# Kernel tuning notes

Measured on AMD Instinct MI355X. Metric: run time of the kernel, lower is better.

## Reference

```python
import jax, jax.numpy as jnp
import numpy as np

N = 2048
EMBED_DIM = 64
N_SUBJ, N_REL, N_OBJ = 16, 9, 16


def setup_inputs() -> dict:
    key = jax.random.key(0)
    ks = jax.random.split(key, 16)
    scale = 0.05  # keep sigmoid unsaturated
    return {
        "subj_idx": jax.random.randint(ks[0], (N,), 0, N_SUBJ, dtype=jnp.int32),
        "rel_idx": jax.random.randint(ks[1], (N,), 0, N_REL, dtype=jnp.int32),
        "obj_idx": jax.random.randint(ks[2], (N,), 0, N_OBJ, dtype=jnp.int32),
        "subj_table": jax.random.normal(ks[3], (N_SUBJ, EMBED_DIM), jnp.float32),
        "rel_table": jax.random.normal(ks[4], (N_REL, EMBED_DIM), jnp.float32),
        "obj_table": jax.random.normal(ks[5], (N_OBJ, EMBED_DIM), jnp.float32),
        "proj_w": jax.random.normal(ks[6], (EMBED_DIM, 3 * EMBED_DIM), jnp.float32) * scale,
        "proj_b": jax.random.normal(ks[7], (EMBED_DIM,), jnp.float32) * scale,
        "w1": jax.random.normal(ks[8], (EMBED_DIM, 2 * EMBED_DIM), jnp.float32) * scale,
        "b1": jax.random.normal(ks[9], (EMBED_DIM,), jnp.float32) * scale,
        "w2": jax.random.normal(ks[10], (32, EMBED_DIM), jnp.float32) * scale,
        "b2": jax.random.normal(ks[11], (32,), jnp.float32) * scale,
        "w3": jax.random.normal(ks[12], (1, 32), jnp.float32) * scale,
        "b3": jax.random.normal(ks[13], (1,), jnp.float32) * scale,
    }


def reference(subj_idx, rel_idx, obj_idx, subj_table, rel_table, obj_table,
              proj_w, proj_b, w1, b1, w2, b2, w3, b3):
    # --- ClaimEmbedder.embed, batched over all N claims ---
    # combined [N, 3*D] = cat(subj, rel, obj) embeddings; proj -> [N, D]
    combined = jnp.concatenate(
        [subj_table[subj_idx], rel_table[rel_idx], obj_table[obj_idx]], axis=-1)
    e = combined @ proj_w.T + proj_b  # [N, D]

    # --- conflict_scorer over all ordered pairs (i, j) ---
    # Linear(2D -> D) on cat(e_i, e_j) == e_i @ W1a.T + e_j @ W1b.T + b1
    d = e.shape[-1]
    w1a, w1b = w1[:, :d], w1[:, d:]
    hi = e @ w1a.T          # [N, D] contribution of left claim
    hj = e @ w1b.T          # [N, D] contribution of right claim
    h = jax.nn.relu(hi[:, None, :] + hj[None, :, :] + b1)  # [N, N, D]
    # Dropout(0.1) is identity in eval / no_grad inference.
    h2 = jax.nn.relu(jnp.einsum('ijd,kd->ijk', h, w2) + b2)  # [N, N, 32]
    scores = jax.nn.sigmoid(jnp.einsum('ijk,k->ij', h2, w3[0]) + b3[0])  # [N, N]
    # Only pairs with i < j are scored in the original nested loop.
    return jnp.triu(scores, k=1)
```

## Files before the change

kernel.cpp:

```cpp
#include <hip/hip_runtime.h>
#include <hip/hip_bf16.h>

#define NROWS 2048

typedef __attribute__((ext_vector_type(4))) float f32x4;
typedef _Float16 f16x2 __attribute__((ext_vector_type(2)));
typedef _Float16 f16x8 __attribute__((ext_vector_type(8)));
typedef __fp16 fp16x2_raw __attribute__((ext_vector_type(2)));

union H8 { f16x8 v; f16x2 h2[4]; };

static __device__ __forceinline__ f32x4 vmax0(f32x4 a) {
    return __builtin_elementwise_max(a, (f32x4)0.f);
}
static __device__ __forceinline__ f16x8 hmax0(f16x8 a) {
    return __builtin_elementwise_max(a, (f16x8)(_Float16)0.f);
}
static __device__ __forceinline__ f16x2 pkrtz(float a, float b) {
    union { fp16x2_raw r; f16x2 f; } c;
    c.r = __builtin_amdgcn_cvt_pkrtz(a, b);
    return c.f;
}

#define TJ_OFF   2688
#define H16_OFF  5376

__global__ __launch_bounds__(256) void tab_kernel(
    const float* __restrict__ subj_table, const float* __restrict__ rel_table,
    const float* __restrict__ obj_table,
    const float* __restrict__ proj_w, const float* __restrict__ proj_b,
    const float* __restrict__ w1, const float* __restrict__ b1,
    float* __restrict__ ws)
{
    __shared__ float et[64];
    const int b = blockIdx.x;
    const int side = b & 1;
    const int r = b >> 1;
    const int tid = threadIdx.x;
    const int lane = tid & 63;
    const int w = tid >> 6;

    if (r == 41) {
        if (tid < 64) et[tid] = proj_b[tid];
    } else {
        const float* src; int off;
        if (r < 16)      { src = subj_table + r * 64;        off = 0;   }
        else if (r < 25) { src = rel_table + (r - 16) * 64;  off = 64;  }
        else             { src = obj_table + (r - 25) * 64;  off = 128; }
        const float sv = src[lane];
        #pragma unroll
        for (int t = 0; t < 4; ++t) {
            const int d0 = w * 16 + t * 4;
            float p0 = sv * proj_w[(d0 + 0) * 192 + off + lane];
            float p1 = sv * proj_w[(d0 + 1) * 192 + off + lane];
            float p2 = sv * proj_w[(d0 + 2) * 192 + off + lane];
            float p3 = sv * proj_w[(d0 + 3) * 192 + off + lane];
            #pragma unroll
            for (int m = 1; m < 64; m <<= 1) {
                p0 += __shfl_xor(p0, m, 64);
                p1 += __shfl_xor(p1, m, 64);
                p2 += __shfl_xor(p2, m, 64);
                p3 += __shfl_xor(p3, m, 64);
            }
            if (lane == 0) {
                et[d0 + 0] = p0; et[d0 + 1] = p1;
                et[d0 + 2] = p2; et[d0 + 3] = p3;
            }
        }
    }
    __syncthreads();

    float* dst = ws + (side ? TJ_OFF : 0);
    const float sv2 = et[lane];
    const int woff = side * 64;
    #pragma unroll
    for (int t = 0; t < 4; ++t) {
        const int d0 = w * 16 + t * 4;
        float p0 = sv2 * w1[(d0 + 0) * 128 + woff + lane];
        float p1 = sv2 * w1[(d0 + 1) * 128 + woff + lane];
        float p2 = sv2 * w1[(d0 + 2) * 128 + woff + lane];
        float p3 = sv2 * w1[(d0 + 3) * 128 + woff + lane];
        #pragma unroll
        for (int m = 1; m < 64; m <<= 1) {
            p0 += __shfl_xor(p0, m, 64);
            p1 += __shfl_xor(p1, m, 64);
            p2 += __shfl_xor(p2, m, 64);
            p3 += __shfl_xor(p3, m, 64);
        }
        if (lane == 0) {
            const bool cst = (side == 0) && (r == 41);
            dst[r * 64 + d0 + 0] = p0 + (cst ? b1[d0 + 0] : 0.f);
            dst[r * 64 + d0 + 1] = p1 + (cst ? b1[d0 + 1] : 0.f);
            dst[r * 64 + d0 + 2] = p2 + (cst ? b1[d0 + 2] : 0.f);
            dst[r * 64 + d0 + 3] = p3 + (cst ? b1[d0 + 3] : 0.f);
        }
    }
}

__global__ __launch_bounds__(256) void hgather_kernel(
    const int* __restrict__ subj_idx, const int* __restrict__ rel_idx,
    const int* __restrict__ obj_idx, float* __restrict__ ws)
{
    _Float16* hi16 = (_Float16*)(ws + H16_OFF);
    _Float16* hj16 = hi16 + NROWS * 64;
    const float* TI = ws;
    const float* TJ = ws + TJ_OFF;

    const int t = threadIdx.x;
    const int n = blockIdx.x * 32 + (t >> 3);
    const int c = (t & 7) * 8;

    const int s = subj_idx[n];
    const int r = 16 + rel_idx[n];
    const int o = 25 + obj_idx[n];

    const f32x4 v0 = *(const f32x4*)(TI + s * 64 + c)
                   + *(const f32x4*)(TI + r * 64 + c)
                   + *(const f32x4*)(TI + o * 64 + c)
                   + *(const f32x4*)(TI + 41 * 64 + c);
    const f32x4 v1 = *(const f32x4*)(TI + s * 64 + c + 4)
                   + *(const f32x4*)(TI + r * 64 + c + 4)
                   + *(const f32x4*)(TI + o * 64 + c + 4)
                   + *(const f32x4*)(TI + 41 * 64 + c + 4);
    H8 hp;
    hp.h2[0] = pkrtz(v0[0], v0[1]); hp.h2[1] = pkrtz(v0[2], v0[3]);
    hp.h2[2] = pkrtz(v1[0], v1[1]); hp.h2[3] = pkrtz(v1[2], v1[3]);
    *(f16x8*)&hi16[(size_t)n * 64 + c] = hp.v;

    const f32x4 u0 = *(const f32x4*)(TJ + s * 64 + c)
                   + *(const f32x4*)(TJ + r * 64 + c)
                   + *(const f32x4*)(TJ + o * 64 + c)
                   + *(const f32x4*)(TJ + 41 * 64 + c);
    const f32x4 u1 = *(const f32x4*)(TJ + s * 64 + c + 4)
                   + *(const f32x4*)(TJ + r * 64 + c + 4)
                   + *(const f32x4*)(TJ + o * 64 + c + 4)
                   + *(const f32x4*)(TJ + 41 * 64 + c + 4);
    H8 hq;
    hq.h2[0] = pkrtz(u0[0], u0[1]); hq.h2[1] = pkrtz(u0[2], u0[3]);
    hq.h2[2] = pkrtz(u1[0], u1[1]); hq.h2[3] = pkrtz(u1[2], u1[3]);
    *(f16x8*)&hj16[(size_t)n * 64 + c] = hq.v;
}

#define PSTR 68

__global__ __launch_bounds__(256, 4) void pair_kernel(
    const float* __restrict__ ws,
    const float* __restrict__ w2, const float* __restrict__ b2,
    const float* __restrict__ w3, const float* __restrict__ b3,
    float* __restrict__ out)
{
    const int bx = blockIdx.x, by = blockIdx.y;
    const int i0 = by * 32, j0 = bx * 32;
    const int tid = threadIdx.x;

    if (bx < by) {
        const float4 z = {0.f, 0.f, 0.f, 0.f};
        ((float4*)(out + (size_t)(i0 + (tid >> 3)) * NROWS + j0))[tid & 7] = z;
        return;
    }

    __shared__ float part[4 * 16 * PSTR];

    const _Float16* hi16 = (const _Float16*)(ws + H16_OFF);
    const _Float16* hj16 = hi16 + NROWS * 64;

    const int lane = tid & 63;
    const int wid  = tid >> 6;
    const int col  = lane & 15;
    const int quad = lane >> 4;
    const int wj   = wid & 1;
    const int wi   = wid >> 1;

    const _Float16* hjr = hj16 + (size_t)(j0 + wj * 16 + col) * 64 + quad * 8;
    const f16x8 hj0 = *(const f16x8*)(hjr);
    const f16x8 hj1 = *(const f16x8*)(hjr + 32);

    H8 wf[2][2];
    #pragma unroll
    for (int ch = 0; ch < 2; ++ch)
        #pragma unroll
        for (int ks = 0; ks < 2; ++ks) {
            const f32x4* wr = (const f32x4*)(w2 + (ch * 16 + col) * 64 + ks * 32 + quad * 8);
            const f32x4 w0 = wr[0], w1v = wr[1];
            wf[ch][ks].h2[0] = pkrtz(w0[0], w0[1]);
            wf[ch][ks].h2[1] = pkrtz(w0[2], w0[3]);
            wf[ch][ks].h2[2] = pkrtz(w1v[0], w1v[1]);
            wf[ch][ks].h2[3] = pkrtz(w1v[2], w1v[3]);
        }
    const f32x4 b2A = *(const f32x4*)(b2 + quad * 4);
    const f32x4 b2B = *(const f32x4*)(b2 + 16 + quad * 4);
    const f32x4 w3A = *(const f32x4*)(w3 + quad * 4);
    const f32x4 w3B = *(const f32x4*)(w3 + 16 + quad * 4);
    const float b3v = b3[0];

    float* mypart = &part[wid * 16 * PSTR];
    const _Float16* hibase = hi16 + (size_t)(i0 + wi * 16) * 64 + quad * 8;

    #pragma unroll 8
    for (int it = 0; it < 16; ++it) {
        const f16x8 x0 = *(const f16x8*)(hibase + it * 64);
        const f16x8 x1 = *(const f16x8*)(hibase + it * 64 + 32);

        const f16x8 f0 = hmax0(x0 + hj0);
        const f16x8 f1 = hmax0(x1 + hj1);

        f32x4 accA = __builtin_amdgcn_mfma_f32_16x16x32_f16(wf[0][0].v, f0, b2A, 0, 0, 0);
        accA       = __builtin_amdgcn_mfma_f32_16x16x32_f16(wf[0][1].v, f1, accA, 0, 0, 0);
        f32x4 accB = __builtin_amdgcn_mfma_f32_16x16x32_f16(wf[1][0].v, f0, b2B, 0, 0, 0);
        accB       = __builtin_amdgcn_mfma_f32_16x16x32_f16(wf[1][1].v, f1, accB, 0, 0, 0);

        const f32x4 ra = vmax0(accA);
        const f32x4 rb = vmax0(accB);
        const f32x4 t4 = ra * w3A + rb * w3B;
        mypart[it * PSTR + quad * 16 + col] = (t4[0] + t4[1]) + (t4[2] + t4[3]);
    }

    {
        const int sub = lane & 3;
        const int itx = lane >> 2;
        const float* pr = &mypart[itx * PSTR + sub * 4];
        const f32x4 s = *(const f32x4*)(pr)
                      + *(const f32x4*)(pr + 16)
                      + *(const f32x4*)(pr + 32)
                      + *(const f32x4*)(pr + 48);
        const int i  = i0 + wi * 16 + itx;
        const int jb = j0 + wj * 16 + sub * 4;
        float4 o;
        o.x = (jb + 0 > i) ? 1.f / (1.f + __expf(-(s[0] + b3v))) : 0.f;
        o.y = (jb + 1 > i) ? 1.f / (1.f + __expf(-(s[1] + b3v))) : 0.f;
        o.z = (jb + 2 > i) ? 1.f / (1.f + __expf(-(s[2] + b3v))) : 0.f;
        o.w = (jb + 3 > i) ? 1.f / (1.f + __expf(-(s[3] + b3v))) : 0.f;
        *(float4*)(out + (size_t)i * NROWS + jb) = o;
    }
}

extern "C" void kernel_launch(void* const* d_in, const int* in_sizes, int n_in,
                              void* d_out, int out_size, void* d_ws, size_t ws_size,
                              hipStream_t stream) {
    const int*   subj_idx   = (const int*)d_in[0];
    const int*   rel_idx    = (const int*)d_in[1];
    const int*   obj_idx    = (const int*)d_in[2];
    const float* subj_table = (const float*)d_in[3];
    const float* rel_table  = (const float*)d_in[4];
    const float* obj_table  = (const float*)d_in[5];
    const float* proj_w     = (const float*)d_in[6];
    const float* proj_b     = (const float*)d_in[7];
    const float* w1         = (const float*)d_in[8];
    const float* b1         = (const float*)d_in[9];
    const float* w2         = (const float*)d_in[10];
    const float* b2         = (const float*)d_in[11];
    const float* w3         = (const float*)d_in[12];
    const float* b3         = (const float*)d_in[13];
    float* out = (float*)d_out;
    float* ws  = (float*)d_ws;

    tab_kernel<<<dim3(84), dim3(256), 0, stream>>>(
        subj_table, rel_table, obj_table, proj_w, proj_b, w1, b1, ws);

    hgather_kernel<<<dim3(NROWS / 32), dim3(256), 0, stream>>>(
        subj_idx, rel_idx, obj_idx, ws);

    pair_kernel<<<dim3(NROWS / 32, NROWS / 32), dim3(256), 0, stream>>>(
        ws, w2, b2, w3, b3, out);
}
```

Baseline: 128.6 us.

## Launch only upper-triangular pair tiles, stage hi/hj in LDS, zero lower tiles separately

The pair kernel now uses a 1D grid of 2080 upper-triangular tile blocks, recovering the tile row and column from the block id with a sqrt-based inverse. Blocks that only wrote zeros are gone. Those zeros come from a separate zfill kernel over the 2016 strictly-lower tiles. Each pair block also stages its 32 hi rows and 32 hj rows in padded LDS instead of reading global memory per wave, and it adds a __syncthreads. The aim is to cut the scheduling overhead of trivial blocks and the redundant global loads, at the cost of one extra kernel launch and a barrier.

Result: faster. 111.6 us (-13.3%).

```diff
diff --git a/kernel.cpp b/kernel.cpp
--- a/kernel.cpp
+++ b/kernel.cpp
@@ -2,6 +2,7 @@
 #include <hip/hip_bf16.h>
 
 #define NROWS 2048
+#define HH 72
 
 typedef __attribute__((ext_vector_type(4))) float f32x4;
 typedef _Float16 f16x2 __attribute__((ext_vector_type(2)));
@@ -141,6 +142,20 @@
     *(f16x8*)&hj16[(size_t)n * 64 + c] = hq.v;
 }
 
+__global__ __launch_bounds__(256) void zfill_kernel(float* __restrict__ out)
+{
+    const int bid = blockIdx.x;
+    int by = (int)((1.f + sqrtf(1.f + 8.f * (float)bid)) * 0.5f);
+    while (by * (by - 1) / 2 > bid) --by;
+    while ((by + 1) * by / 2 <= bid) ++by;
+    const int bx = bid - by * (by - 1) / 2;
+    const int i0 = by * 32, j0 = bx * 32;
+    const int t = threadIdx.x;
+    const int r = t >> 3, c = (t & 7) * 4;
+    const float4 z = {0.f, 0.f, 0.f, 0.f};
+    *(float4*)(out + (size_t)(i0 + r) * NROWS + j0 + c) = z;
+}
+
 #define PSTR 68
 
 __global__ __launch_bounds__(256, 4) void pair_kernel(
@@ -149,16 +164,16 @@
     const float* __restrict__ w3, const float* __restrict__ b3,
     float* __restrict__ out)
 {
-    const int bx = blockIdx.x, by = blockIdx.y;
+    const int bid = blockIdx.x;
+    int by = (int)((129.f - sqrtf(16641.f - 8.f * (float)bid)) * 0.5f);
+    while (by * (129 - by) / 2 > bid) --by;
+    while ((by + 1) * (129 - (by + 1)) / 2 <= bid) ++by;
+    const int bx = by + (bid - by * (129 - by) / 2);
     const int i0 = by * 32, j0 = bx * 32;
     const int tid = threadIdx.x;
 
-    if (bx < by) {
-        const float4 z = {0.f, 0.f, 0.f, 0.f};
-        ((float4*)(out + (size_t)(i0 + (tid >> 3)) * NROWS + j0))[tid & 7] = z;
-        return;
-    }
-
+    __shared__ _Float16 hiL[32 * HH];
+    __shared__ _Float16 hjL[32 * HH];
     __shared__ float part[4 * 16 * PSTR];
 
     const _Float16* hi16 = (const _Float16*)(ws + H16_OFF);
@@ -171,9 +186,12 @@
     const int wj   = wid & 1;
     const int wi   = wid >> 1;
 
-    const _Float16* hjr = hj16 + (size_t)(j0 + wj * 16 + col) * 64 + quad * 8;
-    const f16x8 hj0 = *(const f16x8*)(hjr);
-    const f16x8 hj1 = *(const f16x8*)(hjr + 32);
+    {
+        const int rr = tid >> 3;
+        const int cc = (tid & 7) * 8;
+        *(f16x8*)&hiL[rr * HH + cc] = *(const f16x8*)(hi16 + (size_t)(i0 + rr) * 64 + cc);
+        *(f16x8*)&hjL[rr * HH + cc] = *(const f16x8*)(hj16 + (size_t)(j0 + rr) * 64 + cc);
+    }
 
     H8 wf[2][2];
     #pragma unroll
@@ -193,13 +211,19 @@
     const f32x4 w3B = *(const f32x4*)(w3 + 16 + quad * 4);
     const float b3v = b3[0];
 
+    __syncthreads();
+
+    const int hjb = (wj * 16 + col) * HH + quad * 8;
+    const f16x8 hj0 = *(const f16x8*)&hjL[hjb];
+    const f16x8 hj1 = *(const f16x8*)&hjL[hjb + 32];
+
     float* mypart = &part[wid * 16 * PSTR];
-    const _Float16* hibase = hi16 + (size_t)(i0 + wi * 16) * 64 + quad * 8;
 
     #pragma unroll 8
     for (int it = 0; it < 16; ++it) {
-        const f16x8 x0 = *(const f16x8*)(hibase + it * 64);
-        const f16x8 x1 = *(const f16x8*)(hibase + it * 64 + 32);
+        const int base = (wi * 16 + it) * HH + quad * 8;
+        const f16x8 x0 = *(const f16x8*)&hiL[base];
+        const f16x8 x1 = *(const f16x8*)&hiL[base + 32];
 
         const f16x8 f0 = hmax0(x0 + hj0);
         const f16x8 f1 = hmax0(x1 + hj1);
@@ -254,12 +278,14 @@
     float* out = (float*)d_out;
     float* ws  = (float*)d_ws;
 
+    zfill_kernel<<<dim3(2016), dim3(256), 0, stream>>>(out);
+
     tab_kernel<<<dim3(84), dim3(256), 0, stream>>>(
         subj_table, rel_table, obj_table, proj_w, proj_b, w1, b1, ws);
 
     hgather_kernel<<<dim3(NROWS / 32), dim3(256), 0, stream>>>(
         subj_idx, rel_idx, obj_idx, ws);
 
-    pair_kernel<<<dim3(NROWS / 32, NROWS / 32), dim3(256), 0, stream>>>(
+    pair_kernel<<<dim3(2080), dim3(256), 0, stream>>>(
         ws, w2, b2, w3, b3, out);
 }
```
